# Kernel optimization log

Measured on AMD Instinct MI355X. Metric: run time of the kernel, lower is better.

Reference implementation:

```python
import jax, jax.numpy as jnp
import numpy as np

N = 16384
B = 64
VOCAB = 100
L0 = 128
RADIUS = 8.0
BOX = 50.0


def setup_inputs() -> dict:
    key = jax.random.key(0)
    ks = jax.random.split(key, 8)
    z = jax.random.randint(ks[0], (N,), 0, VOCAB, dtype=jnp.int32)
    batch = jnp.sort(jax.random.randint(ks[1], (N,), 0, B, dtype=jnp.int64))
    pos = jax.random.uniform(ks[2], (N, 3), dtype=jnp.float32) * BOX
    emb = jax.random.normal(ks[3], (VOCAB, L0), dtype=jnp.float32)
    w1 = jax.random.normal(ks[4], (L0, 64), dtype=jnp.float32) * (1.0 / np.sqrt(L0))
    b1 = jnp.zeros((64,), dtype=jnp.float32)
    w2 = jax.random.normal(ks[5], (64, 1), dtype=jnp.float32) * (1.0 / 8.0)
    b2 = jnp.zeros((1,), dtype=jnp.float32)
    return {"z": z, "batch": batch, "pos": pos, "emb": emb,
            "w1": w1, "b1": b1, "w2": w2, "b2": b2}


def _radius_graph_mask(pos, batch, r):
    # Brute-force radius graph (what torch_cluster does without grid binning):
    # pairwise squared distances, thresholded, same-graph, no self-loops.
    # Returns a dense [N, N] bool adjacency mask (fixed shape, jit-friendly).
    sq = jnp.sum(pos * pos, axis=-1)                       # [N]
    d2 = sq[:, None] + sq[None, :] - 2.0 * (pos @ pos.T)   # [N, N]
    same_graph = batch[:, None] == batch[None, :]
    not_self = ~jnp.eye(pos.shape[0], dtype=bool)
    return (d2 < r * r) & same_graph & not_self


def reference(z, batch, pos, emb, w1, b1, w2, b2):
    nodes = emb[z]                                         # [N, L0] embedding lookup
    adj = _radius_graph_mask(pos, batch, RADIUS)           # [N, N] bool
    h = jax.nn.silu(nodes @ w1 + b1)                       # [N, 64]
    out = h @ w2 + b2                                      # [N, 1]
    return out, adj
```

## Files before the change

kernel.cpp:

```cpp
#include <hip/hip_runtime.h>
#include <hip/hip_bf16.h>
#include <math.h>

#define N_NODES 16384
#define TI 32
#define TJ 1024

__global__ __launch_bounds__(256) void detect_i64_kernel(const int* __restrict__ b,
                                                         int* __restrict__ flag) {
    __shared__ int dec;
    if (threadIdx.x == 0) dec = 0;
    __syncthreads();
    int local = 0;
    for (int k = threadIdx.x; k < N_NODES - 1; k += 256)
        if (b[k + 1] < b[k]) local = 1;
    if (local) atomicOr(&dec, 1);
    __syncthreads();
    if (threadIdx.x == 0) flag[0] = dec;
}

__global__ __launch_bounds__(256) void mlp_kernel(const int* __restrict__ z,
                                                  const float* __restrict__ emb,
                                                  const float* __restrict__ w1,
                                                  const float* __restrict__ b1,
                                                  const float* __restrict__ w2,
                                                  const float* __restrict__ b2,
                                                  float* __restrict__ out) {
    const int lane = threadIdx.x & 63;
    const int wave = threadIdx.x >> 6;
    const int i = blockIdx.x * 4 + wave;
    if (i >= N_NODES) return;

    const float4* erow = (const float4*)(emb + (size_t)z[i] * 128);
    float acc = b1[lane];
#pragma unroll 8
    for (int k4 = 0; k4 < 32; k4++) {
        float4 e = erow[k4];
        int k = k4 * 4;
        acc = fmaf(e.x, w1[(k + 0) * 64 + lane], acc);
        acc = fmaf(e.y, w1[(k + 1) * 64 + lane], acc);
        acc = fmaf(e.z, w1[(k + 2) * 64 + lane], acc);
        acc = fmaf(e.w, w1[(k + 3) * 64 + lane], acc);
    }
    float h = acc / (1.0f + expf(-acc));
    float t = h * w2[lane];
#pragma unroll
    for (int off = 32; off >= 1; off >>= 1)
        t += __shfl_xor(t, off, 64);
    if (lane == 0) out[i] = t + b2[0];
}

__global__ __launch_bounds__(256) void adj_kernel(const float* __restrict__ pos,
                                                  const void* __restrict__ batch_raw,
                                                  const int* __restrict__ flag,
                                                  float* __restrict__ adj) {
    __shared__ float s_x[TI], s_y[TI], s_z[TI], s_sq[TI];
    __shared__ int   s_b[TI];

    const bool is64 = (flag[0] != 0);
    const int* b32 = (const int*)batch_raw;
    const long long* b64 = (const long long*)batch_raw;

    const int t     = threadIdx.x;
    const int jbase = blockIdx.x * TJ;
    const int ibase = blockIdx.y * TI;

    if (t < TI) {
        int i = ibase + t;
        float x = pos[i * 3 + 0], y = pos[i * 3 + 1], z = pos[i * 3 + 2];
        s_x[t] = x; s_y[t] = y; s_z[t] = z;
        s_sq[t] = __fadd_rn(__fadd_rn(__fmul_rn(x, x), __fmul_rn(y, y)), __fmul_rn(z, z));
        s_b[t] = is64 ? (int)b64[i] : b32[i];
    }
    __syncthreads();

    const int j0 = jbase + t * 4;
    const float4* p4 = (const float4*)(pos + (size_t)jbase * 3);
    float4 A = p4[t * 3 + 0];
    float4 B = p4[t * 3 + 1];
    float4 C = p4[t * 3 + 2];
    const float xj[4] = {A.x, A.w, B.z, C.y};
    const float yj[4] = {A.y, B.x, B.w, C.z};
    const float zj[4] = {A.z, B.y, C.x, C.w};

    float sqj[4];
#pragma unroll
    for (int m = 0; m < 4; m++)
        sqj[m] = __fadd_rn(__fadd_rn(__fmul_rn(xj[m], xj[m]), __fmul_rn(yj[m], yj[m])),
                           __fmul_rn(zj[m], zj[m]));

    int bj[4];
    if (is64) {
#pragma unroll
        for (int m = 0; m < 4; m++) bj[m] = (int)b64[j0 + m];
    } else {
        int4 bb = *(const int4*)(b32 + j0);
        bj[0] = bb.x; bj[1] = bb.y; bj[2] = bb.z; bj[3] = bb.w;
    }

    float* orow = adj + (size_t)ibase * N_NODES + j0;
#pragma unroll 4
    for (int ii = 0; ii < TI; ii++) {
        const float xi = s_x[ii], yi = s_y[ii], zi = s_z[ii], sqi = s_sq[ii];
        const int bi = s_b[ii];
        const int i = ibase + ii;
        float r[4];
#pragma unroll
        for (int m = 0; m < 4; m++) {
            float dot = fmaf(zi, zj[m], fmaf(yi, yj[m], __fmul_rn(xi, xj[m])));
            float d2 = __fsub_rn(__fadd_rn(sqi, sqj[m]), __fadd_rn(dot, dot));
            bool v = (d2 < 64.0f) && (bi == bj[m]) && (i != j0 + m);
            r[m] = v ? 1.0f : 0.0f;
        }
        float4 rv = make_float4(r[0], r[1], r[2], r[3]);
        *(float4*)(orow + (size_t)ii * N_NODES) = rv;
    }
}

extern "C" void kernel_launch(void* const* d_in, const int* in_sizes, int n_in,
                              void* d_out, int out_size, void* d_ws, size_t ws_size,
                              hipStream_t stream) {
    const int*   z     = (const int*)d_in[0];
    const void*  batch = d_in[1];
    const float* pos   = (const float*)d_in[2];
    const float* emb   = (const float*)d_in[3];
    const float* w1    = (const float*)d_in[4];
    const float* b1    = (const float*)d_in[5];
    const float* w2    = (const float*)d_in[6];
    const float* b2    = (const float*)d_in[7];

    float* out = (float*)d_out;
    float* adj = out + N_NODES;
    int* flag = (int*)d_ws;

    detect_i64_kernel<<<1, 256, 0, stream>>>((const int*)batch, flag);
    mlp_kernel<<<N_NODES / 4, 256, 0, stream>>>(z, emb, w1, b1, w2, b2, out);
    adj_kernel<<<dim3(N_NODES / TJ, N_NODES / TI), 256, 0, stream>>>(pos, batch, flag, adj);
}
```

Baseline: 1.227 ms.

## Use nontemporal adjacency stores, packed LDS, diagonal specialization; fuse dtype check into MLP

The int64 batch-detection kernel is folded into block 0 of the MLP kernel, removing one launch. The adjacency kernel doubles its row tile to 64, packs x/y/z/sq into one vf4 LDS entry, and writes the output with nontemporal stores so the 1 GiB stream does not pollute cache. A templated path drops the self-loop check for tiles that cannot contain the diagonal. The kernel remains bound by writing the dense output, so the gains depend on how much the nontemporal stores help write bandwidth.

```diff
diff --git a/kernel.cpp b/kernel.cpp
--- a/kernel.cpp
+++ b/kernel.cpp
@@ -3,21 +3,10 @@
 #include <math.h>
 
 #define N_NODES 16384
-#define TI 32
+#define TI 64
 #define TJ 1024
 
-__global__ __launch_bounds__(256) void detect_i64_kernel(const int* __restrict__ b,
-                                                         int* __restrict__ flag) {
-    __shared__ int dec;
-    if (threadIdx.x == 0) dec = 0;
-    __syncthreads();
-    int local = 0;
-    for (int k = threadIdx.x; k < N_NODES - 1; k += 256)
-        if (b[k + 1] < b[k]) local = 1;
-    if (local) atomicOr(&dec, 1);
-    __syncthreads();
-    if (threadIdx.x == 0) flag[0] = dec;
-}
+typedef float vf4 __attribute__((ext_vector_type(4)));
 
 __global__ __launch_bounds__(256) void mlp_kernel(const int* __restrict__ z,
                                                   const float* __restrict__ emb,
@@ -25,7 +14,21 @@
                                                   const float* __restrict__ b1,
                                                   const float* __restrict__ w2,
                                                   const float* __restrict__ b2,
+                                                  const int* __restrict__ batch32,
+                                                  int* __restrict__ flag,
                                                   float* __restrict__ out) {
+    if (blockIdx.x == 0) {
+        __shared__ int dec;
+        if (threadIdx.x == 0) dec = 0;
+        __syncthreads();
+        int local = 0;
+        for (int k = threadIdx.x; k < N_NODES - 1; k += 256)
+            if (batch32[k + 1] < batch32[k]) local = 1;
+        if (local) atomicOr(&dec, 1);
+        __syncthreads();
+        if (threadIdx.x == 0) flag[0] = dec;
+    }
+
     const int lane = threadIdx.x & 63;
     const int wave = threadIdx.x >> 6;
     const int i = blockIdx.x * 4 + wave;
@@ -50,12 +53,39 @@
     if (lane == 0) out[i] = t + b2[0];
 }
 
+template <bool DIAG>
+__device__ __forceinline__ void adj_rows(const vf4* __restrict__ s_p,
+                                         const int* __restrict__ s_b,
+                                         const float xj[4], const float yj[4],
+                                         const float zj[4], const float sqj[4],
+                                         const int bj[4],
+                                         int ibase, int j0,
+                                         float* __restrict__ orow) {
+#pragma unroll 4
+    for (int ii = 0; ii < TI; ii++) {
+        vf4 p = s_p[ii];
+        const float xi = p.x, yi = p.y, zi = p.z, sqi = p.w;
+        const int bi = s_b[ii];
+        float r[4];
+#pragma unroll
+        for (int m = 0; m < 4; m++) {
+            float dot = fmaf(zi, zj[m], fmaf(yi, yj[m], __fmul_rn(xi, xj[m])));
+            float d2 = __fsub_rn(__fadd_rn(sqi, sqj[m]), __fadd_rn(dot, dot));
+            bool v = (d2 < 64.0f) && (bi == bj[m]);
+            if (DIAG) v = v && ((ibase + ii) != (j0 + m));
+            r[m] = v ? 1.0f : 0.0f;
+        }
+        vf4 rv = {r[0], r[1], r[2], r[3]};
+        __builtin_nontemporal_store(rv, (vf4*)(orow + (size_t)ii * N_NODES));
+    }
+}
+
 __global__ __launch_bounds__(256) void adj_kernel(const float* __restrict__ pos,
                                                   const void* __restrict__ batch_raw,
                                                   const int* __restrict__ flag,
                                                   float* __restrict__ adj) {
-    __shared__ float s_x[TI], s_y[TI], s_z[TI], s_sq[TI];
-    __shared__ int   s_b[TI];
+    __shared__ vf4 s_p[TI];
+    __shared__ int s_b[TI];
 
     const bool is64 = (flag[0] != 0);
     const int* b32 = (const int*)batch_raw;
@@ -68,8 +98,10 @@
     if (t < TI) {
         int i = ibase + t;
         float x = pos[i * 3 + 0], y = pos[i * 3 + 1], z = pos[i * 3 + 2];
-        s_x[t] = x; s_y[t] = y; s_z[t] = z;
-        s_sq[t] = __fadd_rn(__fadd_rn(__fmul_rn(x, x), __fmul_rn(y, y)), __fmul_rn(z, z));
+        vf4 p;
+        p.x = x; p.y = y; p.z = z;
+        p.w = __fadd_rn(__fadd_rn(__fmul_rn(x, x), __fmul_rn(y, y)), __fmul_rn(z, z));
+        s_p[t] = p;
         s_b[t] = is64 ? (int)b64[i] : b32[i];
     }
     __syncthreads();
@@ -99,22 +131,10 @@
     }
 
     float* orow = adj + (size_t)ibase * N_NODES + j0;
-#pragma unroll 4
-    for (int ii = 0; ii < TI; ii++) {
-        const float xi = s_x[ii], yi = s_y[ii], zi = s_z[ii], sqi = s_sq[ii];
-        const int bi = s_b[ii];
-        const int i = ibase + ii;
-        float r[4];
-#pragma unroll
-        for (int m = 0; m < 4; m++) {
-            float dot = fmaf(zi, zj[m], fmaf(yi, yj[m], __fmul_rn(xi, xj[m])));
-            float d2 = __fsub_rn(__fadd_rn(sqi, sqj[m]), __fadd_rn(dot, dot));
-            bool v = (d2 < 64.0f) && (bi == bj[m]) && (i != j0 + m);
-            r[m] = v ? 1.0f : 0.0f;
-        }
-        float4 rv = make_float4(r[0], r[1], r[2], r[3]);
-        *(float4*)(orow + (size_t)ii * N_NODES) = rv;
-    }
+    if ((unsigned)(ibase - jbase) < (unsigned)TJ)
+        adj_rows<true>(s_p, s_b, xj, yj, zj, sqj, bj, ibase, j0, orow);
+    else
+        adj_rows<false>(s_p, s_b, xj, yj, zj, sqj, bj, ibase, j0, orow);
 }
 
 extern "C" void kernel_launch(void* const* d_in, const int* in_sizes, int n_in,
@@ -133,7 +153,7 @@
     float* adj = out + N_NODES;
     int* flag = (int*)d_ws;
 
-    detect_i64_kernel<<<1, 256, 0, stream>>>((const int*)batch, flag);
-    mlp_kernel<<<N_NODES / 4, 256, 0, stream>>>(z, emb, w1, b1, w2, b2, out);
+    mlp_kernel<<<N_NODES / 4, 256, 0, stream>>>(z, emb, w1, b1, w2, b2,
+                                                (const int*)batch, flag, out);
     adj_kernel<<<dim3(N_NODES / TJ, N_NODES / TI), 256, 0, stream>>>(pos, batch, flag, adj);
 }
```

After: 1.119 ms. 1.1x faster.
